# Performance work log

Hardware: AMD Instinct MI355X
Metric: run time of the kernel (lower is better)

Reference implementation:

```python
import jax, jax.numpy as jnp
import numpy as np
from functools import partial

B, T, H, W, CIN, F = 8, 16, 64, 64, 32, 32
K = 3
BN_EPS = 1e-3


def _conv(x, w):
    # x: [N,H,W,Cin], w: [kh,kw,Cin,Cout], SAME padding, stride 1
    return jax.lax.conv_general_dilated(
        x, w, window_strides=(1, 1), padding='SAME',
        dimension_numbers=('NHWC', 'HWIO', 'NHWC'))


def _hard_sigmoid(x):
    # Keras hard_sigmoid: clip(0.2*x + 0.5, 0, 1)
    return jnp.clip(0.2 * x + 0.5, 0.0, 1.0)


def setup_inputs() -> dict:
    key = jax.random.key(0)
    ks = jax.random.split(key, 4)
    x = jax.random.normal(ks[0], (B, T, H, W, CIN), dtype=jnp.float32)
    Wx = jax.random.normal(ks[1], (K, K, CIN, 4 * F), dtype=jnp.float32) * 0.05
    Wh = jax.random.normal(ks[2], (K, K, F, 4 * F), dtype=jnp.float32) * 0.05
    b = jnp.zeros((4 * F,), dtype=jnp.float32)
    gamma = jnp.ones((F,), dtype=jnp.float32)
    beta = jnp.zeros((F,), dtype=jnp.float32)
    moving_mean = jnp.zeros((F,), dtype=jnp.float32)
    moving_var = jnp.ones((F,), dtype=jnp.float32)
    return {"x": x, "Wx": Wx, "Wh": Wh, "b": b, "gamma": gamma,
            "beta": beta, "moving_mean": moving_mean, "moving_var": moving_var}


def _conv_lstm(x, Wx, Wh, b):
    # Precompute input-to-gate convs for all timesteps at once: [B*T,H,W,4F]
    xg = _conv(x.reshape(B * T, H, W, CIN), Wx) + b
    xg = xg.reshape(B, T, H, W, 4 * F).transpose(1, 0, 2, 3, 4)  # [T,B,H,W,4F]

    def step(carry, xg_t):
        h, c = carry
        g = xg_t + _conv(h, Wh)  # [B,H,W,4F]
        i, f, cc, o = jnp.split(g, 4, axis=-1)  # Keras gate order i,f,c,o
        i = _hard_sigmoid(i)
        f = _hard_sigmoid(f)
        o = _hard_sigmoid(o)
        c = f * c + i * jnp.tanh(cc)
        h = o * jnp.tanh(c)
        return (h, c), h

    h0 = jnp.zeros((B, H, W, F), dtype=x.dtype)
    c0 = jnp.zeros((B, H, W, F), dtype=x.dtype)
    _, hs = jax.lax.scan(step, (h0, c0), xg)  # hs: [T,B,H,W,F]
    return hs.transpose(1, 0, 2, 3, 4)  # [B,T,H,W,F]


def reference(x, Wx, Wh, b, gamma, beta, moving_mean, moving_var):
    y = _conv_lstm(x, Wx, Wh, b)
    # BatchNorm in inference mode (training=False): use moving stats, eps=1e-3
    inv = gamma * jax.lax.rsqrt(moving_var + BN_EPS)
    return y * inv + (beta - moving_mean * inv)
```

## Files before the change

### kernel.cpp

```cpp
#include <hip/hip_runtime.h>
#include <math.h>

#define PSTR 40

typedef _Float16 half8 __attribute__((ext_vector_type(8)));
typedef float    f32x4 __attribute__((ext_vector_type(4)));

__device__ __forceinline__ float fast_tanh(float v) {
    float e = __expf(2.f * v);
    return 1.f - 2.f / (e + 1.f);
}
__device__ __forceinline__ float hsig(float v) {
    return fminf(fmaxf(0.2f * v + 0.5f, 0.f), 1.f);
}

__global__ void prep_w(const float* __restrict__ Wx, const float* __restrict__ Wh,
                       _Float16* __restrict__ Wcx, _Float16* __restrict__ Wch) {
    const int k = blockIdx.x;
    const int n = threadIdx.x;
    const int tap = k >> 6, ci = k & 63;
    if (ci < 32) Wcx[(tap * 128 + n) * 32 + ci]        = (_Float16)Wx[(tap * 32 + ci) * 128 + n];
    else         Wch[(tap * 128 + n) * 32 + (ci - 32)] = (_Float16)Wh[(tap * 32 + (ci - 32)) * 128 + n];
}

__global__ __launch_bounds__(256, 2)
void lstm_step_k(const float* __restrict__ x, const _Float16* __restrict__ Wcx,
                 const _Float16* __restrict__ Wch, const float* __restrict__ bias,
                 const float* __restrict__ gamma_, const float* __restrict__ beta_,
                 const float* __restrict__ mmean, const float* __restrict__ mvar,
                 const _Float16* __restrict__ hprev, _Float16* __restrict__ hnext,
                 float* __restrict__ csw, float* __restrict__ out, int t)
{
    __shared__ _Float16 xp[100 * PSTR];
    __shared__ _Float16 hp[100 * PSTR];

    const int tid  = threadIdx.x;
    const int lane = tid & 63;
    const int w    = tid >> 6;
    const int l15  = lane & 15, quad = lane >> 4;
    const int chg  = w & 1, mtg = w >> 1;
    const int b = blockIdx.x, tx = blockIdx.y, ty = blockIdx.z;
    const int px0 = tx * 8, py0 = ty * 8;
    const int tile = ty * 8 + tx;

    const float* xt = x + (((size_t)b * 16 + t) * 4096) * 32;
    for (int i = tid; i < 400; i += 256) {
        const int pos = i >> 2, q = i & 3;
        const int row = pos / 10, col = pos - row * 10;
        const int gy = py0 + row - 1, gx = px0 + col - 1;
        half8 hv = {0, 0, 0, 0, 0, 0, 0, 0};
        if ((unsigned)gy < 64u && (unsigned)gx < 64u) {
            const float* s = xt + ((size_t)(gy * 64 + gx)) * 32 + q * 8;
            const float4 v0 = *(const float4*)s;
            const float4 v1 = *(const float4*)(s + 4);
            hv = (half8){(_Float16)v0.x, (_Float16)v0.y, (_Float16)v0.z, (_Float16)v0.w,
                         (_Float16)v1.x, (_Float16)v1.y, (_Float16)v1.z, (_Float16)v1.w};
        }
        *(half8*)&xp[pos * PSTR + q * 8] = hv;
    }
    if (t > 0) {
        const _Float16* hb = hprev + (size_t)b * 4096 * 32;
        for (int i = tid; i < 400; i += 256) {
            const int pos = i >> 2, q = i & 3;
            const int row = pos / 10, col = pos - row * 10;
            const int gy = py0 + row - 1, gx = px0 + col - 1;
            half8 hv = {0, 0, 0, 0, 0, 0, 0, 0};
            if ((unsigned)gy < 64u && (unsigned)gx < 64u)
                hv = *(const half8*)(hb + ((size_t)(gy * 64 + gx)) * 32 + q * 8);
            *(half8*)&hp[pos * PSTR + q * 8] = hv;
        }
    }
    __syncthreads();

    const int f = chg * 16 + l15;
    float bi[4];
    #pragma unroll
    for (int nt = 0; nt < 4; ++nt) bi[nt] = bias[nt * 32 + f];
    const float inv = gamma_[f] * rsqrtf(mvar[f] + 1e-3f);
    const float bnb = beta_[f] - mmean[f] * inv;

    f32x4 acc[2][4];
    #pragma unroll
    for (int mt = 0; mt < 2; ++mt)
        #pragma unroll
        for (int nt = 0; nt < 4; ++nt)
            acc[mt][nt] = (f32x4){bi[nt], bi[nt], bi[nt], bi[nt]};

    const int pbase = ((mtg * 4 + (l15 >> 3)) * 10 + (l15 & 7)) * PSTR + quad * 8;
    const _Float16* wbx = Wcx + (chg * 16 + l15) * 32 + quad * 8;

    #pragma unroll
    for (int tap = 0; tap < 9; ++tap) {
        const int ky = tap / 3, kx = tap - ky * 3;
        const half8 a0 = *(const half8*)&xp[pbase + (ky * 10 + kx) * PSTR];
        const half8 a1 = *(const half8*)&xp[pbase + (ky * 10 + kx + 20) * PSTR];
        #pragma unroll
        for (int nt = 0; nt < 4; ++nt) {
            const half8 bf = *(const half8*)(wbx + tap * 4096 + nt * 1024);
            acc[0][nt] = __builtin_amdgcn_mfma_f32_16x16x32_f16(a0, bf, acc[0][nt], 0, 0, 0);
            acc[1][nt] = __builtin_amdgcn_mfma_f32_16x16x32_f16(a1, bf, acc[1][nt], 0, 0, 0);
        }
    }
    if (t > 0) {
        const _Float16* wbh = Wch + (chg * 16 + l15) * 32 + quad * 8;
        #pragma unroll
        for (int tap = 0; tap < 9; ++tap) {
            const int ky = tap / 3, kx = tap - ky * 3;
            const half8 a0 = *(const half8*)&hp[pbase + (ky * 10 + kx) * PSTR];
            const half8 a1 = *(const half8*)&hp[pbase + (ky * 10 + kx + 20) * PSTR];
            #pragma unroll
            for (int nt = 0; nt < 4; ++nt) {
                const half8 bf = *(const half8*)(wbh + tap * 4096 + nt * 1024);
                acc[0][nt] = __builtin_amdgcn_mfma_f32_16x16x32_f16(a0, bf, acc[0][nt], 0, 0, 0);
                acc[1][nt] = __builtin_amdgcn_mfma_f32_16x16x32_f16(a1, bf, acc[1][nt], 0, 0, 0);
            }
        }
    }

    float* cp = csw + (((size_t)b * 64 + tile) * 256 + tid) * 8;
    f32x4 c0 = (f32x4){0.f, 0.f, 0.f, 0.f};
    f32x4 c1 = (f32x4){0.f, 0.f, 0.f, 0.f};
    if (t > 0) {
        c0 = *(const f32x4*)cp;
        c1 = *(const f32x4*)(cp + 4);
    }

    _Float16* hq = hnext + (size_t)b * 4096 * 32;
    float* oq = out + (((size_t)b * 16 + t) * 4096) * 32;
    f32x4 cn0, cn1;
    #pragma unroll
    for (int mt = 0; mt < 2; ++mt) {
        #pragma unroll
        for (int r = 0; r < 4; ++r) {
            const int px = (mtg * 2 + mt) * 16 + quad * 4 + r;
            const int gy = py0 + (px >> 3), gx = px0 + (px & 7);
            const float gi = acc[mt][0][r];
            const float gf = acc[mt][1][r];
            const float gc = acc[mt][2][r];
            const float go = acc[mt][3][r];
            const float co = mt ? c1[r] : c0[r];
            const float cn = hsig(gf) * co + hsig(gi) * fast_tanh(gc);
            const float hv = hsig(go) * fast_tanh(cn);
            if (mt) cn1[r] = cn; else cn0[r] = cn;
            const size_t pix = ((size_t)(gy * 64 + gx)) * 32 + f;
            hq[pix] = (_Float16)hv;
            oq[pix] = hv * inv + bnb;
        }
    }
    *(f32x4*)cp       = cn0;
    *(f32x4*)(cp + 4) = cn1;
}

extern "C" void kernel_launch(void* const* d_in, const int* in_sizes, int n_in,
                              void* d_out, int out_size, void* d_ws, size_t ws_size,
                              hipStream_t stream)
{
    const float* x      = (const float*)d_in[0];
    const float* Wx     = (const float*)d_in[1];
    const float* Wh     = (const float*)d_in[2];
    const float* bias   = (const float*)d_in[3];
    const float* gamma_ = (const float*)d_in[4];
    const float* beta_  = (const float*)d_in[5];
    const float* mmean  = (const float*)d_in[6];
    const float* mvar   = (const float*)d_in[7];
    float* out = (float*)d_out;

    char* wsb = (char*)d_ws;
    _Float16* h0  = (_Float16*)(wsb);
    _Float16* h1  = (_Float16*)(wsb + (1 << 21));
    float*    csw = (float*)(wsb + (1 << 22));
    _Float16* Wcx = (_Float16*)(wsb + (1 << 23));
    _Float16* Wch = (_Float16*)(wsb + (1 << 23) + 73728);

    prep_w<<<dim3(576), dim3(128), 0, stream>>>(Wx, Wh, Wcx, Wch);

    _Float16* hpr = h0;
    _Float16* hnx = h1;
    for (int t = 0; t < 16; ++t) {
        lstm_step_k<<<dim3(8, 8, 8), 256, 0, stream>>>(
            x, Wcx, Wch, bias, gamma_, beta_, mmean, mvar, hpr, hnx, csw, out, t);
        _Float16* tmp = hpr; hpr = hnx; hnx = tmp;
    }
}
```

Measured before the change: 346.7 us.

## Fuse two LSTM timesteps per launch using halo recomputation

Each block now computes two consecutive timesteps. For the first step it works on a 10x10 halo-extended tile (12x12 input halo), keeps the intermediate h and c in shared memory, then computes the second step for the 8x8 interior. This halves the number of kernel launches and global h/c round trips. The cost is redundant halo computation, which raises MFMA work for the first step by roughly half, plus a larger shared memory footprint that may lower occupancy. The cell state layout also changes from per-thread swizzled to pixel-major.

Measured after the change: 347.2 us. Within noise of the previous version (+0.1%).

```diff
diff --git a/kernel.cpp b/kernel.cpp
--- a/kernel.cpp
+++ b/kernel.cpp
@@ -2,6 +2,7 @@
 #include <math.h>
 
 #define PSTR 40
+#define CSTR 33
 
 typedef _Float16 half8 __attribute__((ext_vector_type(8)));
 typedef float    f32x4 __attribute__((ext_vector_type(4)));
@@ -13,6 +14,7 @@
 __device__ __forceinline__ float hsig(float v) {
     return fminf(fmaxf(0.2f * v + 0.5f, 0.f), 1.f);
 }
+__device__ __forceinline__ int div10(int p) { return (p * 205) >> 11; }
 
 __global__ void prep_w(const float* __restrict__ Wx, const float* __restrict__ Wh,
                        _Float16* __restrict__ Wcx, _Float16* __restrict__ Wch) {
@@ -24,15 +26,18 @@
 }
 
 __global__ __launch_bounds__(256, 2)
-void lstm_step_k(const float* __restrict__ x, const _Float16* __restrict__ Wcx,
-                 const _Float16* __restrict__ Wch, const float* __restrict__ bias,
-                 const float* __restrict__ gamma_, const float* __restrict__ beta_,
-                 const float* __restrict__ mmean, const float* __restrict__ mvar,
-                 const _Float16* __restrict__ hprev, _Float16* __restrict__ hnext,
-                 float* __restrict__ csw, float* __restrict__ out, int t)
+void lstm_step2(const float* __restrict__ x, const _Float16* __restrict__ Wcx,
+                const _Float16* __restrict__ Wch, const float* __restrict__ bias,
+                const float* __restrict__ gamma_, const float* __restrict__ beta_,
+                const float* __restrict__ mmean, const float* __restrict__ mvar,
+                const _Float16* __restrict__ hprev, _Float16* __restrict__ hnext,
+                float* __restrict__ csw, float* __restrict__ out, int t)
 {
-    __shared__ _Float16 xp[100 * PSTR];
-    __shared__ _Float16 hp[100 * PSTR];
+    __shared__ _Float16 xpA[160 * PSTR];
+    __shared__ _Float16 hpA[160 * PSTR];
+    __shared__ _Float16 xpB[100 * PSTR];
+    __shared__ _Float16 hpB[112 * PSTR];
+    __shared__ float    cB [112 * CSTR];
 
     const int tid  = threadIdx.x;
     const int lane = tid & 63;
@@ -41,36 +46,49 @@
     const int chg  = w & 1, mtg = w >> 1;
     const int b = blockIdx.x, tx = blockIdx.y, ty = blockIdx.z;
     const int px0 = tx * 8, py0 = ty * 8;
-    const int tile = ty * 8 + tx;
-
-    const float* xt = x + (((size_t)b * 16 + t) * 4096) * 32;
-    for (int i = tid; i < 400; i += 256) {
-        const int pos = i >> 2, q = i & 3;
-        const int row = pos / 10, col = pos - row * 10;
-        const int gy = py0 + row - 1, gx = px0 + col - 1;
+
+    const float* xtA = x + (((size_t)b * 16 + t) * 4096) * 32;
+    for (int i = tid; i < 640; i += 256) {
+        const int cell = i >> 2, q = i & 3;
+        const int row = cell / 12, col = cell - row * 12;
+        const int gy = py0 - 2 + row, gx = px0 - 2 + col;
         half8 hv = {0, 0, 0, 0, 0, 0, 0, 0};
         if ((unsigned)gy < 64u && (unsigned)gx < 64u) {
-            const float* s = xt + ((size_t)(gy * 64 + gx)) * 32 + q * 8;
+            const float* s = xtA + ((size_t)(gy * 64 + gx)) * 32 + q * 8;
             const float4 v0 = *(const float4*)s;
             const float4 v1 = *(const float4*)(s + 4);
             hv = (half8){(_Float16)v0.x, (_Float16)v0.y, (_Float16)v0.z, (_Float16)v0.w,
                          (_Float16)v1.x, (_Float16)v1.y, (_Float16)v1.z, (_Float16)v1.w};
         }
-        *(half8*)&xp[pos * PSTR + q * 8] = hv;
+        *(half8*)&xpA[cell * PSTR + q * 8] = hv;
     }
     if (t > 0) {
         const _Float16* hb = hprev + (size_t)b * 4096 * 32;
-        for (int i = tid; i < 400; i += 256) {
-            const int pos = i >> 2, q = i & 3;
-            const int row = pos / 10, col = pos - row * 10;
-            const int gy = py0 + row - 1, gx = px0 + col - 1;
+        for (int i = tid; i < 640; i += 256) {
+            const int cell = i >> 2, q = i & 3;
+            const int row = cell / 12, col = cell - row * 12;
+            const int gy = py0 - 2 + row, gx = px0 - 2 + col;
             half8 hv = {0, 0, 0, 0, 0, 0, 0, 0};
             if ((unsigned)gy < 64u && (unsigned)gx < 64u)
                 hv = *(const half8*)(hb + ((size_t)(gy * 64 + gx)) * 32 + q * 8);
-            *(half8*)&hp[pos * PSTR + q * 8] = hv;
-        }
-    }
-    __syncthreads();
+            *(half8*)&hpA[cell * PSTR + q * 8] = hv;
+        }
+    }
+    const float* xtB = xtA + (size_t)4096 * 32;
+    for (int i = tid; i < 400; i += 256) {
+        const int cell = i >> 2, q = i & 3;
+        const int row = div10(cell), col = cell - row * 10;
+        const int gy = py0 - 1 + row, gx = px0 - 1 + col;
+        half8 hv = {0, 0, 0, 0, 0, 0, 0, 0};
+        if ((unsigned)gy < 64u && (unsigned)gx < 64u) {
+            const float* s = xtB + ((size_t)(gy * 64 + gx)) * 32 + q * 8;
+            const float4 v0 = *(const float4*)s;
+            const float4 v1 = *(const float4*)(s + 4);
+            hv = (half8){(_Float16)v0.x, (_Float16)v0.y, (_Float16)v0.z, (_Float16)v0.w,
+                         (_Float16)v1.x, (_Float16)v1.y, (_Float16)v1.z, (_Float16)v1.w};
+        }
+        *(half8*)&xpB[cell * PSTR + q * 8] = hv;
+    }
 
     const int f = chg * 16 + l15;
     float bi[4];
@@ -79,76 +97,161 @@
     const float inv = gamma_[f] * rsqrtf(mvar[f] + 1e-3f);
     const float bnb = beta_[f] - mmean[f] * inv;
 
-    f32x4 acc[2][4];
-    #pragma unroll
-    for (int mt = 0; mt < 2; ++mt)
+    const float* cb_g = csw + (size_t)b * 4096 * 32;
+    f32x4 cprev[4];
+    #pragma unroll
+    for (int mt = 0; mt < 4; ++mt) {
+        cprev[mt] = (f32x4){0.f, 0.f, 0.f, 0.f};
+        const int mtile = mt * 2 + mtg;
+        if (t > 0 && mtile < 7) {
+            #pragma unroll
+            for (int r = 0; r < 4; ++r) {
+                const int p = mtile * 16 + quad * 4 + r;
+                const int orow = div10(p), ocol = p - orow * 10;
+                const int gy = py0 - 1 + orow, gx = px0 - 1 + ocol;
+                if ((unsigned)gy < 64u && (unsigned)gx < 64u)
+                    cprev[mt][r] = cb_g[((size_t)(gy * 64 + gx)) * 32 + f];
+            }
+        }
+    }
+
+    __syncthreads();
+
+    f32x4 acc[4][4];
+    #pragma unroll
+    for (int mt = 0; mt < 4; ++mt)
         #pragma unroll
         for (int nt = 0; nt < 4; ++nt)
             acc[mt][nt] = (f32x4){bi[nt], bi[nt], bi[nt], bi[nt]};
 
-    const int pbase = ((mtg * 4 + (l15 >> 3)) * 10 + (l15 & 7)) * PSTR + quad * 8;
+    int qm[4];
+    #pragma unroll
+    for (int mt = 0; mt < 4; ++mt) {
+        const int p = (mt * 2 + mtg) * 16 + l15;
+        qm[mt] = p + 2 * div10(p);
+    }
     const _Float16* wbx = Wcx + (chg * 16 + l15) * 32 + quad * 8;
+    const _Float16* wbh = Wch + (chg * 16 + l15) * 32 + quad * 8;
+    const bool m3 = (mtg == 0);
 
     #pragma unroll
     for (int tap = 0; tap < 9; ++tap) {
         const int ky = tap / 3, kx = tap - ky * 3;
-        const half8 a0 = *(const half8*)&xp[pbase + (ky * 10 + kx) * PSTR];
-        const half8 a1 = *(const half8*)&xp[pbase + (ky * 10 + kx + 20) * PSTR];
+        const int toff = (ky * 12 + kx) * PSTR + quad * 8;
+        half8 ax[4];
+        #pragma unroll
+        for (int mt = 0; mt < 3; ++mt) ax[mt] = *(const half8*)&xpA[qm[mt] * PSTR + toff];
+        ax[3] = m3 ? *(const half8*)&xpA[qm[3] * PSTR + toff] : (half8){0,0,0,0,0,0,0,0};
         #pragma unroll
         for (int nt = 0; nt < 4; ++nt) {
             const half8 bf = *(const half8*)(wbx + tap * 4096 + nt * 1024);
-            acc[0][nt] = __builtin_amdgcn_mfma_f32_16x16x32_f16(a0, bf, acc[0][nt], 0, 0, 0);
-            acc[1][nt] = __builtin_amdgcn_mfma_f32_16x16x32_f16(a1, bf, acc[1][nt], 0, 0, 0);
+            #pragma unroll
+            for (int mt = 0; mt < 4; ++mt)
+                acc[mt][nt] = __builtin_amdgcn_mfma_f32_16x16x32_f16(ax[mt], bf, acc[mt][nt], 0, 0, 0);
         }
     }
     if (t > 0) {
-        const _Float16* wbh = Wch + (chg * 16 + l15) * 32 + quad * 8;
         #pragma unroll
         for (int tap = 0; tap < 9; ++tap) {
             const int ky = tap / 3, kx = tap - ky * 3;
-            const half8 a0 = *(const half8*)&hp[pbase + (ky * 10 + kx) * PSTR];
-            const half8 a1 = *(const half8*)&hp[pbase + (ky * 10 + kx + 20) * PSTR];
+            const int toff = (ky * 12 + kx) * PSTR + quad * 8;
+            half8 ah[4];
+            #pragma unroll
+            for (int mt = 0; mt < 3; ++mt) ah[mt] = *(const half8*)&hpA[qm[mt] * PSTR + toff];
+            ah[3] = m3 ? *(const half8*)&hpA[qm[3] * PSTR + toff] : (half8){0,0,0,0,0,0,0,0};
             #pragma unroll
             for (int nt = 0; nt < 4; ++nt) {
                 const half8 bf = *(const half8*)(wbh + tap * 4096 + nt * 1024);
-                acc[0][nt] = __builtin_amdgcn_mfma_f32_16x16x32_f16(a0, bf, acc[0][nt], 0, 0, 0);
-                acc[1][nt] = __builtin_amdgcn_mfma_f32_16x16x32_f16(a1, bf, acc[1][nt], 0, 0, 0);
+                #pragma unroll
+                for (int mt = 0; mt < 4; ++mt)
+                    acc[mt][nt] = __builtin_amdgcn_mfma_f32_16x16x32_f16(ah[mt], bf, acc[mt][nt], 0, 0, 0);
             }
         }
     }
 
-    float* cp = csw + (((size_t)b * 64 + tile) * 256 + tid) * 8;
-    f32x4 c0 = (f32x4){0.f, 0.f, 0.f, 0.f};
-    f32x4 c1 = (f32x4){0.f, 0.f, 0.f, 0.f};
-    if (t > 0) {
-        c0 = *(const f32x4*)cp;
-        c1 = *(const f32x4*)(cp + 4);
+    float* oqA = out + (((size_t)b * 16 + t) * 4096) * 32;
+    #pragma unroll
+    for (int mt = 0; mt < 4; ++mt) {
+        const int mtile = mt * 2 + mtg;
+        if (mtile < 7) {
+            #pragma unroll
+            for (int r = 0; r < 4; ++r) {
+                const int p = mtile * 16 + quad * 4 + r;
+                const int orow = div10(p), ocol = p - orow * 10;
+                const int gy = py0 - 1 + orow, gx = px0 - 1 + ocol;
+                const bool inimg = ((unsigned)gy < 64u) && ((unsigned)gx < 64u);
+                const float gi = acc[mt][0][r];
+                const float gf = acc[mt][1][r];
+                const float gc = acc[mt][2][r];
+                const float go = acc[mt][3][r];
+                float cn = hsig(gf) * cprev[mt][r] + hsig(gi) * fast_tanh(gc);
+                float hv = hsig(go) * fast_tanh(cn);
+                if (!inimg) { cn = 0.f; hv = 0.f; }
+                hpB[p * PSTR + f] = (_Float16)hv;
+                cB [p * CSTR + f] = cn;
+                if ((unsigned)(orow - 1) < 8u && (unsigned)(ocol - 1) < 8u)
+                    oqA[((size_t)(gy * 64 + gx)) * 32 + f] = hv * inv + bnb;
+            }
+        }
+    }
+
+    __syncthreads();
+
+    f32x4 accB[2][4];
+    #pragma unroll
+    for (int mtb = 0; mtb < 2; ++mtb)
+        #pragma unroll
+        for (int nt = 0; nt < 4; ++nt)
+            accB[mtb][nt] = (f32x4){bi[nt], bi[nt], bi[nt], bi[nt]};
+
+    int q8[2];
+    #pragma unroll
+    for (int mtb = 0; mtb < 2; ++mtb) {
+        const int p8 = (mtg * 2 + mtb) * 16 + l15;
+        q8[mtb] = p8 + 2 * (p8 >> 3);
+    }
+    #pragma unroll
+    for (int tap = 0; tap < 9; ++tap) {
+        const int ky = tap / 3, kx = tap - ky * 3;
+        const int toff = (ky * 10 + kx) * PSTR + quad * 8;
+        const half8 ax0 = *(const half8*)&xpB[q8[0] * PSTR + toff];
+        const half8 ax1 = *(const half8*)&xpB[q8[1] * PSTR + toff];
+        const half8 ah0 = *(const half8*)&hpB[q8[0] * PSTR + toff];
+        const half8 ah1 = *(const half8*)&hpB[q8[1] * PSTR + toff];
+        #pragma unroll
+        for (int nt = 0; nt < 4; ++nt) {
+            const half8 bfx = *(const half8*)(wbx + tap * 4096 + nt * 1024);
+            const half8 bfh = *(const half8*)(wbh + tap * 4096 + nt * 1024);
+            accB[0][nt] = __builtin_amdgcn_mfma_f32_16x16x32_f16(ax0, bfx, accB[0][nt], 0, 0, 0);
+            accB[1][nt] = __builtin_amdgcn_mfma_f32_16x16x32_f16(ax1, bfx, accB[1][nt], 0, 0, 0);
+            accB[0][nt] = __builtin_amdgcn_mfma_f32_16x16x32_f16(ah0, bfh, accB[0][nt], 0, 0, 0);
+            accB[1][nt] = __builtin_amdgcn_mfma_f32_16x16x32_f16(ah1, bfh, accB[1][nt], 0, 0, 0);
+        }
     }
 
     _Float16* hq = hnext + (size_t)b * 4096 * 32;
-    float* oq = out + (((size_t)b * 16 + t) * 4096) * 32;
-    f32x4 cn0, cn1;
-    #pragma unroll
-    for (int mt = 0; mt < 2; ++mt) {
+    float* cq = csw + (size_t)b * 4096 * 32;
+    float* oqB = out + (((size_t)b * 16 + t + 1) * 4096) * 32;
+    #pragma unroll
+    for (int mtb = 0; mtb < 2; ++mtb) {
         #pragma unroll
         for (int r = 0; r < 4; ++r) {
-            const int px = (mtg * 2 + mt) * 16 + quad * 4 + r;
-            const int gy = py0 + (px >> 3), gx = px0 + (px & 7);
-            const float gi = acc[mt][0][r];
-            const float gf = acc[mt][1][r];
-            const float gc = acc[mt][2][r];
-            const float go = acc[mt][3][r];
-            const float co = mt ? c1[r] : c0[r];
-            const float cn = hsig(gf) * co + hsig(gi) * fast_tanh(gc);
+            const int p8 = (mtg * 2 + mtb) * 16 + quad * 4 + r;
+            const int orow8 = p8 >> 3, ocol8 = p8 & 7;
+            const float ct = cB[(p8 + 2 * orow8 + 11) * CSTR + f];
+            const float gi = accB[mtb][0][r];
+            const float gf = accB[mtb][1][r];
+            const float gc = accB[mtb][2][r];
+            const float go = accB[mtb][3][r];
+            const float cn = hsig(gf) * ct + hsig(gi) * fast_tanh(gc);
             const float hv = hsig(go) * fast_tanh(cn);
-            if (mt) cn1[r] = cn; else cn0[r] = cn;
+            const int gy = py0 + orow8, gx = px0 + ocol8;
             const size_t pix = ((size_t)(gy * 64 + gx)) * 32 + f;
             hq[pix] = (_Float16)hv;
-            oq[pix] = hv * inv + bnb;
-        }
-    }
-    *(f32x4*)cp       = cn0;
-    *(f32x4*)(cp + 4) = cn1;
+            cq[pix] = cn;
+            oqB[pix] = hv * inv + bnb;
+        }
+    }
 }
 
 extern "C" void kernel_launch(void* const* d_in, const int* in_sizes, int n_in,
@@ -176,9 +279,9 @@
 
     _Float16* hpr = h0;
     _Float16* hnx = h1;
-    for (int t = 0; t < 16; ++t) {
-        lstm_step_k<<<dim3(8, 8, 8), 256, 0, stream>>>(
-            x, Wcx, Wch, bias, gamma_, beta_, mmean, mvar, hpr, hnx, csw, out, t);
+    for (int tp = 0; tp < 8; ++tp) {
+        lstm_step2<<<dim3(8, 8, 8), 256, 0, stream>>>(
+            x, Wcx, Wch, bias, gamma_, beta_, mmean, mvar, hpr, hnx, csw, out, 2 * tp);
         _Float16* tmp = hpr; hpr = hnx; hnx = tmp;
     }
 }
```

## Assign one gate per wave and stage gate results through LDS for vectorized epilogue

Applied to the files above, without the earlier changes.

Each wave now computes one gate (i, f, c or o) for all 64 pixels of the tile, instead of splitting by channel half and pixel half. That lets each A fragment be reused across two N tiles and each B fragment across four M tiles. The accumulators are written to a padded shared-memory buffer, and after a barrier each thread combines the four gates for 8 contiguous channels of one pixel. This gives vectorized 16-byte stores for h, out and the cell state instead of scattered scalar writes. The cost is an extra ~36KB of LDS per block, which may reduce occupancy, plus an additional barrier and a shared-memory round trip.

New measurement: 293.0 us. 1.18x faster.

```diff
diff --git a/kernel.cpp b/kernel.cpp
--- a/kernel.cpp
+++ b/kernel.cpp
@@ -2,6 +2,8 @@
 #include <math.h>
 
 #define PSTR 40
+#define GSTR 35
+#define GPL  (64 * GSTR)
 
 typedef _Float16 half8 __attribute__((ext_vector_type(8)));
 typedef float    f32x4 __attribute__((ext_vector_type(4)));
@@ -33,12 +35,12 @@
 {
     __shared__ _Float16 xp[100 * PSTR];
     __shared__ _Float16 hp[100 * PSTR];
+    __shared__ float    glds[4 * GPL];
 
     const int tid  = threadIdx.x;
     const int lane = tid & 63;
     const int w    = tid >> 6;
     const int l15  = lane & 15, quad = lane >> 4;
-    const int chg  = w & 1, mtg = w >> 1;
     const int b = blockIdx.x, tx = blockIdx.y, ty = blockIdx.z;
     const int px0 = tx * 8, py0 = ty * 8;
     const int tile = ty * 8 + tx;
@@ -70,85 +72,121 @@
             *(half8*)&hp[pos * PSTR + q * 8] = hv;
         }
     }
+
+    const float bi0 = bias[w * 32 + l15];
+    const float bi1 = bias[w * 32 + 16 + l15];
+
     __syncthreads();
 
-    const int f = chg * 16 + l15;
-    float bi[4];
-    #pragma unroll
-    for (int nt = 0; nt < 4; ++nt) bi[nt] = bias[nt * 32 + f];
-    const float inv = gamma_[f] * rsqrtf(mvar[f] + 1e-3f);
-    const float bnb = beta_[f] - mmean[f] * inv;
-
-    f32x4 acc[2][4];
-    #pragma unroll
-    for (int mt = 0; mt < 2; ++mt)
-        #pragma unroll
-        for (int nt = 0; nt < 4; ++nt)
-            acc[mt][nt] = (f32x4){bi[nt], bi[nt], bi[nt], bi[nt]};
-
-    const int pbase = ((mtg * 4 + (l15 >> 3)) * 10 + (l15 & 7)) * PSTR + quad * 8;
-    const _Float16* wbx = Wcx + (chg * 16 + l15) * 32 + quad * 8;
+    f32x4 acc[4][2];
+    #pragma unroll
+    for (int mt = 0; mt < 4; ++mt) {
+        acc[mt][0] = (f32x4){bi0, bi0, bi0, bi0};
+        acc[mt][1] = (f32x4){bi1, bi1, bi1, bi1};
+    }
+
+    int pb[4];
+    #pragma unroll
+    for (int mt = 0; mt < 4; ++mt) {
+        const int p = mt * 16 + l15;
+        pb[mt] = ((mt * 2 + (l15 >> 3)) * 10 + (l15 & 7)) * PSTR + quad * 8;
+    }
+    const _Float16* wbx = Wcx + ((size_t)(w * 32 + l15)) * 32 + quad * 8;
+    const _Float16* wbh = Wch + ((size_t)(w * 32 + l15)) * 32 + quad * 8;
 
     #pragma unroll
     for (int tap = 0; tap < 9; ++tap) {
         const int ky = tap / 3, kx = tap - ky * 3;
-        const half8 a0 = *(const half8*)&xp[pbase + (ky * 10 + kx) * PSTR];
-        const half8 a1 = *(const half8*)&xp[pbase + (ky * 10 + kx + 20) * PSTR];
-        #pragma unroll
-        for (int nt = 0; nt < 4; ++nt) {
-            const half8 bf = *(const half8*)(wbx + tap * 4096 + nt * 1024);
-            acc[0][nt] = __builtin_amdgcn_mfma_f32_16x16x32_f16(a0, bf, acc[0][nt], 0, 0, 0);
-            acc[1][nt] = __builtin_amdgcn_mfma_f32_16x16x32_f16(a1, bf, acc[1][nt], 0, 0, 0);
+        const int toff = (ky * 10 + kx) * PSTR;
+        half8 a[4];
+        #pragma unroll
+        for (int mt = 0; mt < 4; ++mt) a[mt] = *(const half8*)&xp[pb[mt] + toff];
+        #pragma unroll
+        for (int ntl = 0; ntl < 2; ++ntl) {
+            const half8 bf = *(const half8*)(wbx + tap * 4096 + ntl * 512);
+            #pragma unroll
+            for (int mt = 0; mt < 4; ++mt)
+                acc[mt][ntl] = __builtin_amdgcn_mfma_f32_16x16x32_f16(a[mt], bf, acc[mt][ntl], 0, 0, 0);
         }
     }
     if (t > 0) {
-        const _Float16* wbh = Wch + (chg * 16 + l15) * 32 + quad * 8;
         #pragma unroll
         for (int tap = 0; tap < 9; ++tap) {
             const int ky = tap / 3, kx = tap - ky * 3;
-            const half8 a0 = *(const half8*)&hp[pbase + (ky * 10 + kx) * PSTR];
-            const half8 a1 = *(const half8*)&hp[pbase + (ky * 10 + kx + 20) * PSTR];
-            #pragma unroll
-            for (int nt = 0; nt < 4; ++nt) {
-                const half8 bf = *(const half8*)(wbh + tap * 4096 + nt * 1024);
-                acc[0][nt] = __builtin_amdgcn_mfma_f32_16x16x32_f16(a0, bf, acc[0][nt], 0, 0, 0);
-                acc[1][nt] = __builtin_amdgcn_mfma_f32_16x16x32_f16(a1, bf, acc[1][nt], 0, 0, 0);
+            const int toff = (ky * 10 + kx) * PSTR;
+            half8 a[4];
+            #pragma unroll
+            for (int mt = 0; mt < 4; ++mt) a[mt] = *(const half8*)&hp[pb[mt] + toff];
+            #pragma unroll
+            for (int ntl = 0; ntl < 2; ++ntl) {
+                const half8 bf = *(const half8*)(wbh + tap * 4096 + ntl * 512);
+                #pragma unroll
+                for (int mt = 0; mt < 4; ++mt)
+                    acc[mt][ntl] = __builtin_amdgcn_mfma_f32_16x16x32_f16(a[mt], bf, acc[mt][ntl], 0, 0, 0);
             }
         }
     }
 
+    #pragma unroll
+    for (int mt = 0; mt < 4; ++mt)
+        #pragma unroll
+        for (int ntl = 0; ntl < 2; ++ntl)
+            #pragma unroll
+            for (int r = 0; r < 4; ++r) {
+                const int px = mt * 16 + quad * 4 + r;
+                glds[w * GPL + px * GSTR + ntl * 16 + l15] = acc[mt][ntl][r];
+            }
+
+    __syncthreads();
+
+    const int pxt = tid >> 2, f0 = (tid & 3) * 8;
+    const int gy = py0 + (pxt >> 3), gx = px0 + (pxt & 7);
+
+    float gav[8], bev[8], mmv[8], mvv[8];
+    *(float4*)&gav[0] = *(const float4*)&gamma_[f0];
+    *(float4*)&gav[4] = *(const float4*)&gamma_[f0 + 4];
+    *(float4*)&bev[0] = *(const float4*)&beta_[f0];
+    *(float4*)&bev[4] = *(const float4*)&beta_[f0 + 4];
+    *(float4*)&mmv[0] = *(const float4*)&mmean[f0];
+    *(float4*)&mmv[4] = *(const float4*)&mmean[f0 + 4];
+    *(float4*)&mvv[0] = *(const float4*)&mvar[f0];
+    *(float4*)&mvv[4] = *(const float4*)&mvar[f0 + 4];
+
     float* cp = csw + (((size_t)b * 64 + tile) * 256 + tid) * 8;
-    f32x4 c0 = (f32x4){0.f, 0.f, 0.f, 0.f};
-    f32x4 c1 = (f32x4){0.f, 0.f, 0.f, 0.f};
+    float cov[8];
+    #pragma unroll
+    for (int j = 0; j < 8; ++j) cov[j] = 0.f;
     if (t > 0) {
-        c0 = *(const f32x4*)cp;
-        c1 = *(const f32x4*)(cp + 4);
-    }
-
+        *(f32x4*)&cov[0] = *(const f32x4*)cp;
+        *(f32x4*)&cov[4] = *(const f32x4*)(cp + 4);
+    }
+
+    const int gb = pxt * GSTR + f0;
+    half8 hv8;
+    float ov[8], cnv[8];
+    #pragma unroll
+    for (int j = 0; j < 8; ++j) {
+        const float gi = glds[0 * GPL + gb + j];
+        const float gf = glds[1 * GPL + gb + j];
+        const float gc = glds[2 * GPL + gb + j];
+        const float go = glds[3 * GPL + gb + j];
+        const float inv = gav[j] * rsqrtf(mvv[j] + 1e-3f);
+        const float bnb = bev[j] - mmv[j] * inv;
+        const float cn = hsig(gf) * cov[j] + hsig(gi) * fast_tanh(gc);
+        const float hh = hsig(go) * fast_tanh(cn);
+        cnv[j] = cn;
+        hv8[j] = (_Float16)hh;
+        ov[j] = hh * inv + bnb;
+    }
+
+    const size_t pix = ((size_t)(gy * 64 + gx)) * 32 + f0;
     _Float16* hq = hnext + (size_t)b * 4096 * 32;
     float* oq = out + (((size_t)b * 16 + t) * 4096) * 32;
-    f32x4 cn0, cn1;
-    #pragma unroll
-    for (int mt = 0; mt < 2; ++mt) {
-        #pragma unroll
-        for (int r = 0; r < 4; ++r) {
-            const int px = (mtg * 2 + mt) * 16 + quad * 4 + r;
-            const int gy = py0 + (px >> 3), gx = px0 + (px & 7);
-            const float gi = acc[mt][0][r];
-            const float gf = acc[mt][1][r];
-            const float gc = acc[mt][2][r];
-            const float go = acc[mt][3][r];
-            const float co = mt ? c1[r] : c0[r];
-            const float cn = hsig(gf) * co + hsig(gi) * fast_tanh(gc);
-            const float hv = hsig(go) * fast_tanh(cn);
-            if (mt) cn1[r] = cn; else cn0[r] = cn;
-            const size_t pix = ((size_t)(gy * 64 + gx)) * 32 + f;
-            hq[pix] = (_Float16)hv;
-            oq[pix] = hv * inv + bnb;
-        }
-    }
-    *(f32x4*)cp       = cn0;
-    *(f32x4*)(cp + 4) = cn1;
+    *(half8*)(hq + pix) = hv8;
+    *(float4*)(oq + pix)     = *(float4*)&ov[0];
+    *(float4*)(oq + pix + 4) = *(float4*)&ov[4];
+    *(f32x4*)cp       = *(f32x4*)&cnv[0];
+    *(f32x4*)(cp + 4) = *(f32x4*)&cnv[4];
 }
 
 extern "C" void kernel_launch(void* const* d_in, const int* in_sizes, int n_in,
```
